# Kernel tuning notes

Measured on AMD Instinct MI355X. Metric: run time of the kernel, lower is better.

## Reference

```python
import jax, jax.numpy as jnp
import numpy as np

# dims
V, D, H = 30000, 300, 300
NS, L = 10000, 32
B, NMAX, MMAX = 256, 128, 128
EPS = 0.1          # sinkhorn entropic regularizer
ITERS = 50         # fixed sinkhorn sweeps (replaces convergence check, jit-friendly)
NEG = 1e9
PAD = 0


def setup_inputs() -> dict:
    key = jax.random.key(0)
    ks = jax.random.split(key, 12)
    data = jax.random.randint(ks[0], (NS, L), 0, V, dtype=jnp.int32)
    row_idx = jax.random.randint(ks[1], (B, NMAX), 0, NS, dtype=jnp.int32)
    col_idx = jax.random.randint(ks[2], (B, MMAX), 0, NS, dtype=jnp.int32)
    row_len = jax.random.randint(ks[3], (B,), 1, NMAX + 1, dtype=jnp.int32)
    col_len = jax.random.randint(ks[4], (B,), 1, MMAX + 1, dtype=jnp.int32)
    g = lambda k, shape, fan: (jax.random.normal(k, shape, jnp.float32) / np.sqrt(fan)).astype(jnp.float32)
    return {
        'data': data, 'row_idx': row_idx, 'col_idx': col_idx,
        'row_len': row_len, 'col_len': col_len,
        'emb': g(ks[5], (V, D), D),
        'W1': g(ks[6], (D, H), D), 'b1': jnp.zeros((H,), jnp.float32),
        'W2': g(ks[7], (H, H), H), 'b2': jnp.zeros((H,), jnp.float32),
        'Wc': g(ks[8], (2 * H, H), 2 * H), 'bc': jnp.zeros((H,), jnp.float32),
        'Wcls': g(ks[9], (2 * H, H), 2 * H), 'bcls': jnp.zeros((H,), jnp.float32),
        'Wout': g(ks[10], (H, 2), H), 'bout': jnp.zeros((2,), jnp.float32),
    }


def _forward(data, row_idx, col_idx, row_len, col_len,
             emb, W1, b1, W2, b2, Wc, bc, Wcls, bcls, Wout, bout):
    # ---- Embedder: token embedding + masked mean pool over tokens ----
    tok = emb[data]                                        # [NS, L, D]
    tmask = (data != PAD).astype(tok.dtype)[..., None]     # [NS, L, 1]
    enc = (tok * tmask).sum(1) / jnp.clip(tmask.sum(1), 1.0)   # [NS, D]
    # ---- attention_forward: 2-layer FFN ----
    henc = jax.nn.relu(jax.nn.relu(enc @ W1 + b1) @ W2 + b2)   # [NS, H]
    # ---- variable-length gather + pad (scope) ----
    rows = henc[row_idx]                                   # [B, NMAX, H]
    cols = henc[col_idx]                                   # [B, MMAX, H]
    rmask = (jnp.arange(NMAX)[None, :] < row_len[:, None]).astype(henc.dtype)
    cmask = (jnp.arange(MMAX)[None, :] < col_len[:, None]).astype(henc.dtype)
    rows = rows * rmask[..., None]
    cols = cols * cmask[..., None]
    # ---- batched pairwise cosine cost ----
    rn = rows / (jnp.linalg.norm(rows, axis=-1, keepdims=True) + 1e-8)
    cn = cols / (jnp.linalg.norm(cols, axis=-1, keepdims=True) + 1e-8)
    C = 1.0 - jnp.einsum('bnd,bmd->bnm', rn, cn)           # [B, NMAX, MMAX]
    pmask = rmask[:, :, None] * cmask[:, None, :]
    Cm = jnp.where(pmask > 0, C, 1e4)
    # uniform marginals over valid rows/cols (log-domain, -inf -> -NEG on pads)
    loga = jnp.where(rmask > 0, -jnp.log(row_len.astype(C.dtype))[:, None], -NEG)
    logb = jnp.where(cmask > 0, -jnp.log(col_len.astype(C.dtype))[:, None], -NEG)
    # ---- log-domain Sinkhorn (row/col marginal rescaling) ----
    def step(carry, _):
        f, g = carry
        f = EPS * loga - EPS * jax.nn.logsumexp((g[:, None, :] - Cm) / EPS, axis=2)
        g = EPS * logb - EPS * jax.nn.logsumexp((f[:, :, None] - Cm) / EPS, axis=1)
        return (f, g), None
    (f, g), _ = jax.lax.scan(step, (jnp.zeros_like(loga), jnp.zeros_like(logb)), None, length=ITERS)
    P = jnp.exp((f[:, :, None] + g[:, None, :] - Cm) / EPS) * pmask  # [B, NMAX, MMAX]
    # ---- attend: column_alignments @ rows, row_alignments @ columns ----
    attended_row = jnp.einsum('bnm,bnd->bmd', P, rows)     # P^T @ rows
    attended_col = jnp.einsum('bnm,bmd->bnd', P, cols)     # P @ cols
    # ---- compare_forward (1 layer) + masked sum ----
    cr = jax.nn.relu(jnp.concatenate([rows, attended_col], -1) @ Wc + bc)
    cr = (cr * rmask[..., None]).sum(1)                    # [B, H]
    cc = jax.nn.relu(jnp.concatenate([cols, attended_row], -1) @ Wc + bc)
    cc = (cc * cmask[..., None]).sum(1)                    # [B, H]
    # ---- cls_forward + out ----
    z = jax.nn.relu(jnp.concatenate([cr, cc], -1) @ Wcls + bcls)
    return z @ Wout + bout                                 # [B, 2]


def reference(data, row_idx, col_idx, row_len, col_len,
              emb, W1, b1, W2, b2, Wc, bc, Wcls, bcls, Wout, bout):
    return _forward(data, row_idx, col_idx, row_len, col_len,
                    emb, W1, b1, W2, b2, Wc, bc, Wcls, bcls, Wout, bout)
```

## Files before the change

kernel.cpp:

```cpp
#include <hip/hip_runtime.h>
#include <math.h>

#define NS 10000
#define LSEQ 32
#define DDIM 300
#define HDIM 300
#define BB 256
#define NMAX 128
#define MMAX 128
#define EPSR 0.1f
#define SITERS 50
#define KPAD 320
#define NPADW 384

typedef __attribute__((ext_vector_type(8))) short bf16x8;
typedef __attribute__((ext_vector_type(4))) float f32x4;

__device__ __forceinline__ ushort f2bf(float x) {
  union { float f; unsigned u; } c; c.f = x;
  unsigned r = (c.u + 0x7fffu + ((c.u >> 16) & 1u)) >> 16;
  return (ushort)r;
}
__device__ __forceinline__ float bf2f(ushort h) {
  union { unsigned u; float f; } c; c.u = ((unsigned)h) << 16;
  return c.f;
}

__global__ __launch_bounds__(256) void k_embed(const int* __restrict__ data,
                                               const float* __restrict__ emb,
                                               ushort* __restrict__ enchi,
                                               ushort* __restrict__ enclo) {
  int wv = threadIdx.x >> 6, lane = threadIdx.x & 63;
  int s = blockIdx.x * 4 + wv;
  int myid = (lane < LSEQ) ? data[s * LSEQ + lane] : 0;
  unsigned long long bal = __ballot(lane < LSEQ && myid != 0);
  int cnt = __popcll(bal);
  const float4* emb4 = (const float4*)emb;
  float4 a0 = make_float4(0.f, 0.f, 0.f, 0.f);
  float4 a1 = make_float4(0.f, 0.f, 0.f, 0.f);
#pragma unroll
  for (int t = 0; t < LSEQ; ++t) {
    int id = __shfl(myid, t, 64);
    float m = (id != 0) ? 1.f : 0.f;
    float4 e0 = emb4[(size_t)id * 75 + lane];
    a0.x += e0.x * m; a0.y += e0.y * m; a0.z += e0.z * m; a0.w += e0.w * m;
    if (lane < 11) {
      float4 e1 = emb4[(size_t)id * 75 + 64 + lane];
      a1.x += e1.x * m; a1.y += e1.y * m; a1.z += e1.z * m; a1.w += e1.w * m;
    }
  }
  float inv = 1.f / (float)(cnt > 0 ? cnt : 1);
  size_t base = (size_t)s * KPAD;
  {
    float v0 = a0.x * inv, v1 = a0.y * inv, v2 = a0.z * inv, v3 = a0.w * inv;
    ushort4 h, l;
    h.x = f2bf(v0); l.x = f2bf(v0 - bf2f(h.x));
    h.y = f2bf(v1); l.y = f2bf(v1 - bf2f(h.y));
    h.z = f2bf(v2); l.z = f2bf(v2 - bf2f(h.z));
    h.w = f2bf(v3); l.w = f2bf(v3 - bf2f(h.w));
    *(ushort4*)&enchi[base + lane * 4] = h;
    *(ushort4*)&enclo[base + lane * 4] = l;
  }
  if (lane < 11) {
    float v0 = a1.x * inv, v1 = a1.y * inv, v2 = a1.z * inv, v3 = a1.w * inv;
    ushort4 h, l;
    h.x = f2bf(v0); l.x = f2bf(v0 - bf2f(h.x));
    h.y = f2bf(v1); l.y = f2bf(v1 - bf2f(h.y));
    h.z = f2bf(v2); l.z = f2bf(v2 - bf2f(h.z));
    h.w = f2bf(v3); l.w = f2bf(v3 - bf2f(h.w));
    *(ushort4*)&enchi[base + 256 + lane * 4] = h;
    *(ushort4*)&enclo[base + 256 + lane * 4] = l;
  } else if (lane < 16) {
    ushort4 z; z.x = z.y = z.z = z.w = 0;
    *(ushort4*)&enchi[base + 300 + (lane - 11) * 4] = z;
    *(ushort4*)&enclo[base + 300 + (lane - 11) * 4] = z;
  }
}

__global__ __launch_bounds__(256) void k_cvt_all(
    const float* __restrict__ W1, const float* __restrict__ W2,
    const float* __restrict__ Wc, ushort* __restrict__ W1hi,
    ushort* __restrict__ W1lo, ushort* __restrict__ W2hi,
    ushort* __restrict__ W2lo, ushort* __restrict__ Wchi,
    ushort* __restrict__ Wclo) {
  int i = blockIdx.x * 256 + threadIdx.x;
  const int SA = NPADW * KPAD;
  const int SC = 640 * KPAD;
  float v = 0.f;
  ushort *ph, *pl;
  int idx;
  if (i < SA) {
    idx = i;
    int n = idx / KPAD, k = idx - n * KPAD;
    if (n < HDIM && k < DDIM) v = W1[(size_t)k * HDIM + n];
    ph = W1hi; pl = W1lo;
  } else if (i < 2 * SA) {
    idx = i - SA;
    int n = idx / KPAD, k = idx - n * KPAD;
    if (n < HDIM && k < HDIM) v = W2[(size_t)k * HDIM + n];
    ph = W2hi; pl = W2lo;
  } else if (i < 2 * SA + SC) {
    idx = i - 2 * SA;
    int n = idx / KPAD, k = idx - n * KPAD;
    if (k < HDIM && n < 2 * HDIM)
      v = (n < HDIM) ? Wc[(size_t)k * HDIM + n]
                     : Wc[(size_t)(HDIM + k) * HDIM + (n - HDIM)];
    ph = Wchi; pl = Wclo;
  } else {
    return;
  }
  ushort h = f2bf(v);
  ph[idx] = h;
  pl[idx] = f2bf(v - bf2f(h));
}

__global__ __launch_bounds__(256) void k_gemm_mfma(
    const ushort* __restrict__ Ahi, const ushort* __restrict__ Alo,
    const ushort* __restrict__ BhiT, const ushort* __restrict__ BloT,
    const float* __restrict__ bias, int M, int N, int relu,
    float* __restrict__ Cf, ushort* __restrict__ Chi,
    ushort* __restrict__ Clo) {
  __shared__ __align__(16) ushort ldsA[2][64][40];
  __shared__ __align__(16) ushort ldsB[2][128][40];
  int tid = threadIdx.x;
  int m0 = blockIdx.x * 64, n0 = blockIdx.y * 128;
  int rowA = tid >> 2, chA = (tid & 3) * 8;
  int rowB = tid >> 1, chB = (tid & 1) * 16;
  bool mok = (m0 + rowA) < M;
  const ushort* pAh = Ahi + (size_t)(m0 + rowA) * KPAD + chA;
  const ushort* pAl = Alo + (size_t)(m0 + rowA) * KPAD + chA;
  const ushort* pBh = BhiT + (size_t)(n0 + rowB) * KPAD + chB;
  const ushort* pBl = BloT + (size_t)(n0 + rowB) * KPAD + chB;
  uint4 rAh, rAl, rBh0, rBh1, rBl0, rBl1;
  uint4 z4; z4.x = z4.y = z4.z = z4.w = 0;
  auto ld = [&](int c) {
    int o = c * 32;
    rAh = mok ? *(const uint4*)(pAh + o) : z4;
    rAl = mok ? *(const uint4*)(pAl + o) : z4;
    rBh0 = *(const uint4*)(pBh + o);
    rBh1 = *(const uint4*)(pBh + o + 8);
    rBl0 = *(const uint4*)(pBl + o);
    rBl1 = *(const uint4*)(pBl + o + 8);
  };
  auto st = [&]() {
    *(uint4*)&ldsA[0][rowA][chA] = rAh;
    *(uint4*)&ldsA[1][rowA][chA] = rAl;
    *(uint4*)&ldsB[0][rowB][chB] = rBh0;
    *(uint4*)&ldsB[0][rowB][chB + 8] = rBh1;
    *(uint4*)&ldsB[1][rowB][chB] = rBl0;
    *(uint4*)&ldsB[1][rowB][chB + 8] = rBl1;
  };
  int w = tid >> 6, lane = tid & 63;
  int q = lane >> 4, l16 = lane & 15;
  int mh = w >> 1, nh = w & 1;
  f32x4 zf = {0.f, 0.f, 0.f, 0.f};
  f32x4 acc[2][4];
#pragma unroll
  for (int s = 0; s < 2; ++s)
#pragma unroll
    for (int t = 0; t < 4; ++t) acc[s][t] = zf;
  ld(0); st(); __syncthreads();
  for (int c = 0; c < 10; ++c) {
    if (c < 9) ld(c + 1);
    bf16x8 ah0 = *(const bf16x8*)&ldsA[0][mh * 32 + l16][q * 8];
    bf16x8 ah1 = *(const bf16x8*)&ldsA[0][mh * 32 + 16 + l16][q * 8];
    bf16x8 al0 = *(const bf16x8*)&ldsA[1][mh * 32 + l16][q * 8];
    bf16x8 al1 = *(const bf16x8*)&ldsA[1][mh * 32 + 16 + l16][q * 8];
#pragma unroll
    for (int t = 0; t < 4; ++t) {
      int brow = nh * 64 + t * 16 + l16;
      bf16x8 bh = *(const bf16x8*)&ldsB[0][brow][q * 8];
      bf16x8 bl = *(const bf16x8*)&ldsB[1][brow][q * 8];
      acc[0][t] = __builtin_amdgcn_mfma_f32_16x16x32_bf16(ah0, bh, acc[0][t], 0, 0, 0);
      acc[0][t] = __builtin_amdgcn_mfma_f32_16x16x32_bf16(ah0, bl, acc[0][t], 0, 0, 0);
      acc[0][t] = __builtin_amdgcn_mfma_f32_16x16x32_bf16(al0, bh, acc[0][t], 0, 0, 0);
      acc[1][t] = __builtin_amdgcn_mfma_f32_16x16x32_bf16(ah1, bh, acc[1][t], 0, 0, 0);
      acc[1][t] = __builtin_amdgcn_mfma_f32_16x16x32_bf16(ah1, bl, acc[1][t], 0, 0, 0);
      acc[1][t] = __builtin_amdgcn_mfma_f32_16x16x32_bf16(al1, bh, acc[1][t], 0, 0, 0);
    }
    __syncthreads();
    if (c < 9) st();
    __syncthreads();
  }
#pragma unroll
  for (int t = 0; t < 4; ++t) {
    int n = n0 + nh * 64 + t * 16 + l16;
    bool nin = n < N;
    float bz = (bias && nin) ? bias[n] : 0.f;
#pragma unroll
    for (int s = 0; s < 2; ++s) {
#pragma unroll
      for (int r = 0; r < 4; ++r) {
        int m = m0 + mh * 32 + s * 16 + q * 4 + r;
        if (m >= M) continue;
        float v = acc[s][t][r] + bz;
        if (relu) v = v > 0.f ? v : 0.f;
        if (Cf && nin) Cf[(size_t)m * N + n] = v;
        if (Chi && n < KPAD) {
          ushort h = 0, l = 0;
          if (nin) { h = f2bf(v); l = f2bf(v - bf2f(h)); }
          Chi[(size_t)m * KPAD + n] = h;
          Clo[(size_t)m * KPAD + n] = l;
        }
      }
    }
  }
}

__global__ __launch_bounds__(256) void k_norm_split(
    const ushort* __restrict__ hehi, const ushort* __restrict__ helo,
    ushort* __restrict__ hnhi, ushort* __restrict__ hnlo) {
  int s = blockIdx.x * 4 + (threadIdx.x >> 6);
  int lane = threadIdx.x & 63;
  if (s >= NS) return;
  const ushort* ph = hehi + (size_t)s * KPAD;
  const ushort* pl = helo + (size_t)s * KPAD;
  float x[5];
  float ss = 0.f;
#pragma unroll
  for (int q = 0; q < 5; ++q) {
    int d = lane + q * 64;
    x[q] = bf2f(ph[d]) + bf2f(pl[d]);
    ss += x[q] * x[q];
  }
#pragma unroll
  for (int off = 32; off > 0; off >>= 1) ss += __shfl_down(ss, off, 64);
  ss = __shfl(ss, 0, 64);
  float inv = 1.f / (sqrtf(ss) + 1e-8f);
  ushort* qh = hnhi + (size_t)s * KPAD;
  ushort* ql = hnlo + (size_t)s * KPAD;
#pragma unroll
  for (int q = 0; q < 5; ++q) {
    int d = lane + q * 64;
    float v = x[q] * inv;
    ushort h = f2bf(v);
    qh[d] = h;
    ql[d] = f2bf(v - bf2f(h));
  }
}

__global__ __launch_bounds__(256) void k_cost_mfma(
    const ushort* __restrict__ hnhi, const ushort* __restrict__ hnlo,
    const int* __restrict__ ridx, const int* __restrict__ cidx,
    const int* __restrict__ rlen, const int* __restrict__ clen,
    float* __restrict__ Kmat) {
  int b = blockIdx.z;
  int r0 = blockIdx.x * 64, c0 = blockIdx.y * 64;
  int rl = rlen[b], cl = clen[b];
  float* Kg = Kmat + (size_t)b * NMAX * MMAX;
  int tid = threadIdx.x;
  if (r0 >= rl || c0 >= cl) {
    for (int l = tid; l < 64 * 16; l += 256) {
      int i = l >> 4, j = (l & 15) << 2;
      *(float4*)&Kg[(size_t)(r0 + i) * MMAX + c0 + j] =
          make_float4(0.f, 0.f, 0.f, 0.f);
    }
    return;
  }
  __shared__ int rix[64], cix[64];
  __shared__ __align__(16) ushort lds[4][64][40];
  if (tid < 64) rix[tid] = ridx[b * NMAX + r0 + tid];
  else if (tid < 128) cix[tid - 64] = cidx[b * MMAX + c0 + tid - 64];
  __syncthreads();
  int row = tid >> 2, ch = tid & 3;
  const ushort* pRh = hnhi + (size_t)rix[row] * KPAD + ch * 8;
  const ushort* pRl = hnlo + (size_t)rix[row] * KPAD + ch * 8;
  const ushort* pCh = hnhi + (size_t)cix[row] * KPAD + ch * 8;
  const ushort* pCl = hnlo + (size_t)cix[row] * KPAD + ch * 8;
  uint4 rRh, rRl, rCh, rCl;
  auto ld = [&](int c) {
    int o = c * 32;
    rRh = *(const uint4*)(pRh + o);
    rRl = *(const uint4*)(pRl + o);
    rCh = *(const uint4*)(pCh + o);
    rCl = *(const uint4*)(pCl + o);
  };
  auto st = [&]() {
    *(uint4*)&lds[0][row][ch * 8] = rRh;
    *(uint4*)&lds[1][row][ch * 8] = rRl;
    *(uint4*)&lds[2][row][ch * 8] = rCh;
    *(uint4*)&lds[3][row][ch * 8] = rCl;
  };
  int w = tid >> 6, lane = tid & 63;
  int q = lane >> 4, l16 = lane & 15;
  int mh = w >> 1, nh = w & 1;
  f32x4 zf = {0.f, 0.f, 0.f, 0.f};
  f32x4 acc[2][2];
#pragma unroll
  for (int s = 0; s < 2; ++s)
#pragma unroll
    for (int t = 0; t < 2; ++t) acc[s][t] = zf;
  ld(0); st(); __syncthreads();
  for (int c = 0; c < 10; ++c) {
    if (c < 9) ld(c + 1);
    bf16x8 ah0 = *(const bf16x8*)&lds[0][mh * 32 + l16][q * 8];
    bf16x8 ah1 = *(const bf16x8*)&lds[0][mh * 32 + 16 + l16][q * 8];
    bf16x8 al0 = *(const bf16x8*)&lds[1][mh * 32 + l16][q * 8];
    bf16x8 al1 = *(const bf16x8*)&lds[1][mh * 32 + 16 + l16][q * 8];
#pragma unroll
    for (int t = 0; t < 2; ++t) {
      int brow = nh * 32 + t * 16 + l16;
      bf16x8 bh = *(const bf16x8*)&lds[2][brow][q * 8];
      bf16x8 bl = *(const bf16x8*)&lds[3][brow][q * 8];
      acc[0][t] = __builtin_amdgcn_mfma_f32_16x16x32_bf16(ah0, bh, acc[0][t], 0, 0, 0);
      acc[0][t] = __builtin_amdgcn_mfma_f32_16x16x32_bf16(ah0, bl, acc[0][t], 0, 0, 0);
      acc[0][t] = __builtin_amdgcn_mfma_f32_16x16x32_bf16(al0, bh, acc[0][t], 0, 0, 0);
      acc[1][t] = __builtin_amdgcn_mfma_f32_16x16x32_bf16(ah1, bh, acc[1][t], 0, 0, 0);
      acc[1][t] = __builtin_amdgcn_mfma_f32_16x16x32_bf16(ah1, bl, acc[1][t], 0, 0, 0);
      acc[1][t] = __builtin_amdgcn_mfma_f32_16x16x32_bf16(al1, bh, acc[1][t], 0, 0, 0);
    }
    __syncthreads();
    if (c < 9) st();
    __syncthreads();
  }
#pragma unroll
  for (int t = 0; t < 2; ++t) {
    int n = c0 + nh * 32 + t * 16 + l16;
#pragma unroll
    for (int s = 0; s < 2; ++s) {
#pragma unroll
      for (int r = 0; r < 4; ++r) {
        int m = r0 + mh * 32 + s * 16 + q * 4 + r;
        float kv = (m < rl && n < cl) ? expf((acc[s][t][r] - 1.f) / EPSR) : 0.f;
        Kg[(size_t)m * MMAX + n] = kv;
      }
    }
  }
}

__global__ __launch_bounds__(512) void k_sinkhorn(
    float* __restrict__ Kmat, const int* __restrict__ rlen,
    const int* __restrict__ clen, ushort* __restrict__ Phi,
    ushort* __restrict__ Plo, ushort* __restrict__ PThi,
    ushort* __restrict__ PTlo) {
  __shared__ __align__(16) float vq[4][36];
  __shared__ __align__(16) float uq[4][36];
  int b = blockIdx.x;
  int tid = threadIdx.x;
  int n = tid >> 2, q = tid & 3;
  int rl = rlen[b], cl = clen[b];
  float* Kg = Kmat + (size_t)b * NMAX * MMAX;
  float kr[32], kt[32];
  const float4* Kg4 = (const float4*)(Kg + (size_t)n * MMAX + 32 * q);
#pragma unroll
  for (int t = 0; t < 8; ++t) *(float4*)&kr[4 * t] = Kg4[t];
#pragma unroll
  for (int j = 0; j < 32; ++j) kt[j] = Kg[(size_t)(32 * q + j) * MMAX + n];
  if (tid < 128) vq[tid >> 5][tid & 31] = (tid < cl) ? 1.f : 0.f;
  float av = (n < rl) ? 1.f / (float)rl : 0.f;
  float bv = (n < cl) ? 1.f / (float)cl : 0.f;
  float un = 0.f;
  __syncthreads();
  for (int it = 0; it < SITERS; ++it) {
    float s = 0.f;
#pragma unroll
    for (int t = 0; t < 8; ++t) {
      float4 vv = *(const float4*)&vq[q][4 * t];
      s += kr[4 * t + 0] * vv.x + kr[4 * t + 1] * vv.y +
           kr[4 * t + 2] * vv.z + kr[4 * t + 3] * vv.w;
    }
    s += __shfl_xor(s, 1, 64);
    s += __shfl_xor(s, 2, 64);
    un = (n < rl) ? av / s : 0.f;
    if (q == 0) uq[n >> 5][n & 31] = un;
    __syncthreads();
    float s2 = 0.f;
#pragma unroll
    for (int t = 0; t < 8; ++t) {
      float4 uu = *(const float4*)&uq[q][4 * t];
      s2 += kt[4 * t + 0] * uu.x + kt[4 * t + 1] * uu.y +
            kt[4 * t + 2] * uu.z + kt[4 * t + 3] * uu.w;
    }
    s2 += __shfl_xor(s2, 1, 64);
    s2 += __shfl_xor(s2, 2, 64);
    float vm = (n < cl) ? bv / s2 : 0.f;
    if (q == 0) vq[n >> 5][n & 31] = vm;
    __syncthreads();
  }
  float vn = vq[n >> 5][n & 31];
  size_t rowoff = (size_t)b * (NMAX * MMAX) + (size_t)n * MMAX + 32 * q;
  {
    uint hw[16], lw[16];
#pragma unroll
    for (int t = 0; t < 16; ++t) {
      float p0 = un * kr[2 * t] * vq[q][2 * t];
      float p1 = un * kr[2 * t + 1] * vq[q][2 * t + 1];
      ushort h0 = f2bf(p0), h1 = f2bf(p1);
      hw[t] = (uint)h0 | ((uint)h1 << 16);
      lw[t] = (uint)f2bf(p0 - bf2f(h0)) | ((uint)f2bf(p1 - bf2f(h1)) << 16);
    }
#pragma unroll
    for (int t4 = 0; t4 < 4; ++t4) {
      uint4 vh = make_uint4(hw[4 * t4], hw[4 * t4 + 1], hw[4 * t4 + 2], hw[4 * t4 + 3]);
      uint4 vl = make_uint4(lw[4 * t4], lw[4 * t4 + 1], lw[4 * t4 + 2], lw[4 * t4 + 3]);
      *(uint4*)(Phi + rowoff + 8 * t4) = vh;
      *(uint4*)(Plo + rowoff + 8 * t4) = vl;
    }
  }
  {
    uint hw[16], lw[16];
#pragma unroll
    for (int t = 0; t < 16; ++t) {
      float p0 = uq[q][2 * t] * kt[2 * t] * vn;
      float p1 = uq[q][2 * t + 1] * kt[2 * t + 1] * vn;
      ushort h0 = f2bf(p0), h1 = f2bf(p1);
      hw[t] = (uint)h0 | ((uint)h1 << 16);
      lw[t] = (uint)f2bf(p0 - bf2f(h0)) | ((uint)f2bf(p1 - bf2f(h1)) << 16);
    }
#pragma unroll
    for (int t4 = 0; t4 < 4; ++t4) {
      uint4 vh = make_uint4(hw[4 * t4], hw[4 * t4 + 1], hw[4 * t4 + 2], hw[4 * t4 + 3]);
      uint4 vl = make_uint4(lw[4 * t4], lw[4 * t4 + 1], lw[4 * t4 + 2], lw[4 * t4 + 3]);
      *(uint4*)(PThi + rowoff + 8 * t4) = vh;
      *(uint4*)(PTlo + rowoff + 8 * t4) = vl;
    }
  }
}

__global__ __launch_bounds__(256) void k_att_mfma(
    const ushort* __restrict__ Phi, const ushort* __restrict__ Plo,
    const ushort* __restrict__ PThi, const ushort* __restrict__ PTlo,
    const float* __restrict__ HcB, const int* __restrict__ row_idx,
    const int* __restrict__ col_idx, const int* __restrict__ row_len,
    const int* __restrict__ col_len, const float* __restrict__ bc,
    float* __restrict__ cr, float* __restrict__ cc) {
  int b = blockIdx.y;
  int side = blockIdx.z;
  int c0 = blockIdx.x * 64;
  const int* idx_main = side == 0 ? row_idx : col_idx;
  const int* idx_other = side == 0 ? col_idx : row_idx;
  int lm = side == 0 ? row_len[b] : col_len[b];
  int lo = side == 0 ? col_len[b] : row_len[b];
  const ushort* Ah = (side == 0 ? Phi : PThi) + (size_t)b * (NMAX * MMAX);
  const ushort* Al = (side == 0 ? Plo : PTlo) + (size_t)b * (NMAX * MMAX);
  float* outacc = side == 0 ? cr : cc;

  __shared__ __align__(16) ushort gldh[64][128];
  __shared__ __align__(16) ushort gldl[64][128];
  __shared__ float red[4][64];
  __shared__ int iox[NMAX];
  __shared__ int imx[NMAX];

  int tid = threadIdx.x;
  int w = tid >> 6, lane = tid & 63;
  int q = lane >> 4, l16 = lane & 15;
  if (tid < 128) iox[tid] = idx_other[b * NMAX + tid];
  else imx[tid - 128] = idx_main[b * NMAX + tid - 128];
  __syncthreads();

  int nkc = (lo + 31) >> 5;
  int ndt = (300 - c0 + 15) >> 4;
  if (ndt > 4) ndt = 4;
  bool dok = (c0 + lane) < 300;

  int i0a = w * 16;
  int i0b = 64 + w * 16;
  bool act0 = i0a < lm;
  bool act1 = i0b < lm;

  float gv[32];
#pragma unroll
  for (int t = 0; t < 32; ++t) {
    int k = w * 32 + t;
    gv[t] = (k < lo && dok) ? HcB[(size_t)iox[k] * 600 + 300 + c0 + lane]
                            : 0.f;
  }
  float mpre[2][4][4];
#pragma unroll
  for (int s = 0; s < 2; ++s) {
    int ib = ((s == 0) ? i0a : i0b) + q * 4;
#pragma unroll
    for (int r = 0; r < 4; ++r) {
      int i = ib + r;
      int hrow = imx[i];
#pragma unroll
      for (int dt = 0; dt < 4; ++dt) {
        int col = c0 + dt * 16 + l16;
        mpre[s][r][dt] =
            (i < lm && col < 300) ? HcB[(size_t)hrow * 600 + col] : 0.f;
      }
    }
  }
  float bcv[4];
#pragma unroll
  for (int dt = 0; dt < 4; ++dt) {
    int col = c0 + dt * 16 + l16;
    bcv[dt] = (col < 300) ? bc[col] : 0.f;
  }

  if (w < nkc) {
#pragma unroll
    for (int blk = 0; blk < 4; ++blk) {
      int kb8 = 4 * w + blk;
      int phys = kb8 ^ (lane & 15);
      ushort hb[8], lb[8];
#pragma unroll
      for (int e = 0; e < 8; ++e) {
        float v = gv[blk * 8 + e];
        ushort h = f2bf(v);
        hb[e] = h;
        lb[e] = f2bf(v - bf2f(h));
      }
      *(uint4*)&gldh[lane][phys * 8] = *(uint4*)hb;
      *(uint4*)&gldl[lane][phys * 8] = *(uint4*)lb;
    }
  }
  __syncthreads();

  f32x4 zf = {0.f, 0.f, 0.f, 0.f};
  f32x4 acc0[4], acc1[4];
#pragma unroll
  for (int dt = 0; dt < 4; ++dt) { acc0[dt] = zf; acc1[dt] = zf; }

#pragma unroll 1
  for (int ch = 0; ch < 2; ++ch) {
    if (ch * 2 >= nkc) break;
    bf16x8 f0h[2], f0l[2], f1h[2], f1l[2];
#pragma unroll
    for (int u = 0; u < 2; ++u) {
      int c = ch * 2 + u;
      if (c < nkc) {
        size_t oa = (size_t)(i0a + l16) * MMAX + 32 * c + 8 * q;
        size_t ob = (size_t)(i0b + l16) * MMAX + 32 * c + 8 * q;
        if (act0) {
          f0h[u] = *(const bf16x8*)&Ah[oa];
          f0l[u] = *(const bf16x8*)&Al[oa];
        }
        if (act1) {
          f1h[u] = *(const bf16x8*)&Ah[ob];
          f1l[u] = *(const bf16x8*)&Al[ob];
        }
      }
    }
#pragma unroll
    for (int u = 0; u < 2; ++u) {
      int c = ch * 2 + u;
      if (c < nkc) {
        int phys = (4 * c + q) ^ l16;
#pragma unroll
        for (int dt = 0; dt < 4; ++dt) {
          if (dt < ndt) {
            int d = dt * 16 + l16;
            bf16x8 bh = *(const bf16x8*)&gldh[d][phys * 8];
            bf16x8 bl = *(const bf16x8*)&gldl[d][phys * 8];
            if (act0) {
              acc0[dt] = __builtin_amdgcn_mfma_f32_16x16x32_bf16(f0h[u], bh, acc0[dt], 0, 0, 0);
              acc0[dt] = __builtin_amdgcn_mfma_f32_16x16x32_bf16(f0h[u], bl, acc0[dt], 0, 0, 0);
              acc0[dt] = __builtin_amdgcn_mfma_f32_16x16x32_bf16(f0l[u], bh, acc0[dt], 0, 0, 0);
            }
            if (act1) {
              acc1[dt] = __builtin_amdgcn_mfma_f32_16x16x32_bf16(f1h[u], bh, acc1[dt], 0, 0, 0);
              acc1[dt] = __builtin_amdgcn_mfma_f32_16x16x32_bf16(f1h[u], bl, acc1[dt], 0, 0, 0);
              acc1[dt] = __builtin_amdgcn_mfma_f32_16x16x32_bf16(f1l[u], bh, acc1[dt], 0, 0, 0);
            }
          }
        }
      }
    }
  }

  float psum[4] = {0.f, 0.f, 0.f, 0.f};
#pragma unroll
  for (int s = 0; s < 2; ++s) {
    bool act = (s == 0) ? act0 : act1;
    if (!act) continue;
    int ibase = ((s == 0) ? i0a : i0b) + q * 4;
#pragma unroll
    for (int r = 0; r < 4; ++r) {
      int i = ibase + r;
      if (i >= lm) continue;
#pragma unroll
      for (int dt = 0; dt < 4; ++dt) {
        int col = c0 + dt * 16 + l16;
        if (dt < ndt && col < 300) {
          float av = (s == 0) ? acc0[dt][r] : acc1[dt][r];
          float y = av + mpre[s][r][dt] + bcv[dt];
          psum[dt] += y > 0.f ? y : 0.f;
        }
      }
    }
  }
#pragma unroll
  for (int dt = 0; dt < 4; ++dt) {
    psum[dt] += __shfl_xor(psum[dt], 16, 64);
    psum[dt] += __shfl_xor(psum[dt], 32, 64);
  }
  if (lane < 16) {
#pragma unroll
    for (int dt = 0; dt < 4; ++dt) red[w][dt * 16 + lane] = psum[dt];
  }
  __syncthreads();
  if (tid < 64) {
    float s = red[0][tid] + red[1][tid] + red[2][tid] + red[3][tid];
    int col = c0 + tid;
    if (col < 300) outacc[(size_t)b * HDIM + col] = s;
  }
}

__global__ __launch_bounds__(320) void k_cls(
    const float* __restrict__ cr, const float* __restrict__ cc,
    const float* __restrict__ Wcls, const float* __restrict__ bcls,
    const float* __restrict__ Wout, const float* __restrict__ bout,
    float* __restrict__ out) {
  __shared__ __align__(16) float cz[2 * HDIM];
  __shared__ float zz[HDIM];
  int b = blockIdx.x, tid = threadIdx.x;
  if (tid < HDIM) {
    cz[tid] = cr[(size_t)b * HDIM + tid];
    cz[HDIM + tid] = cc[(size_t)b * HDIM + tid];
  }
  __syncthreads();
  if (tid < HDIM) {
    float acc = bcls[tid];
    for (int k4 = 0; k4 < 2 * HDIM; k4 += 4) {
      float4 c = *(const float4*)&cz[k4];
      acc += c.x * Wcls[(size_t)(k4 + 0) * HDIM + tid] +
             c.y * Wcls[(size_t)(k4 + 1) * HDIM + tid] +
             c.z * Wcls[(size_t)(k4 + 2) * HDIM + tid] +
             c.w * Wcls[(size_t)(k4 + 3) * HDIM + tid];
    }
    zz[tid] = acc > 0.f ? acc : 0.f;
  }
  __syncthreads();
  int o = tid >> 6, lane = tid & 63;
  if (o < 2) {
    float p = 0.f;
    for (int j = lane; j < HDIM; j += 64) p += zz[j] * Wout[(size_t)j * 2 + o];
#pragma unroll
    for (int off = 32; off > 0; off >>= 1) p += __shfl_down(p, off, 64);
    if (lane == 0) out[b * 2 + o] = p + bout[o];
  }
}

extern "C" void kernel_launch(void* const* d_in, const int* in_sizes, int n_in,
                              void* d_out, int out_size, void* d_ws, size_t ws_size,
                              hipStream_t stream) {
  (void)in_sizes; (void)n_in; (void)out_size; (void)ws_size;
  const int* data = (const int*)d_in[0];
  const int* row_idx = (const int*)d_in[1];
  const int* col_idx = (const int*)d_in[2];
  const int* row_len = (const int*)d_in[3];
  const int* col_len = (const int*)d_in[4];
  const float* emb = (const float*)d_in[5];
  const float* W1 = (const float*)d_in[6];
  const float* b1 = (const float*)d_in[7];
  const float* W2 = (const float*)d_in[8];
  const float* b2 = (const float*)d_in[9];
  const float* Wc = (const float*)d_in[10];
  const float* bc = (const float*)d_in[11];
  const float* Wcls = (const float*)d_in[12];
  const float* bcls = (const float*)d_in[13];
  const float* Wout = (const float*)d_in[14];
  const float* bout = (const float*)d_in[15];
  float* out = (float*)d_out;

  char* wp = (char*)d_ws;
  auto carve = [&](size_t bytes) {
    char* p = wp; wp += (bytes + 255) & ~(size_t)255; return p;
  };
  ushort* enchi = (ushort*)carve((size_t)NS * KPAD * 2);
  ushort* enclo = (ushort*)carve((size_t)NS * KPAD * 2);
  ushort* h1hi = (ushort*)carve((size_t)NS * KPAD * 2);
  ushort* h1lo = (ushort*)carve((size_t)NS * KPAD * 2);
  ushort* hehi = (ushort*)carve((size_t)NS * KPAD * 2);
  ushort* helo = (ushort*)carve((size_t)NS * KPAD * 2);
  ushort* hnhi = (ushort*)carve((size_t)NS * KPAD * 2);
  ushort* hnlo = (ushort*)carve((size_t)NS * KPAD * 2);
  ushort* W1hi = (ushort*)carve((size_t)NPADW * KPAD * 2);
  ushort* W1lo = (ushort*)carve((size_t)NPADW * KPAD * 2);
  ushort* W2hi = (ushort*)carve((size_t)NPADW * KPAD * 2);
  ushort* W2lo = (ushort*)carve((size_t)NPADW * KPAD * 2);
  ushort* Wchi = (ushort*)carve((size_t)640 * KPAD * 2);
  ushort* Wclo = (ushort*)carve((size_t)640 * KPAD * 2);
  float* HcB = (float*)carve((size_t)NS * 600 * 4);
  float* Km = (float*)carve((size_t)BB * NMAX * MMAX * 4);
  float* cr = (float*)carve((size_t)BB * HDIM * 4);
  float* cc = (float*)carve((size_t)BB * HDIM * 4);

  ushort* Phi = enchi;
  ushort* Plo = h1hi;
  ushort* PThi = hehi;
  ushort* PTlo = hnhi;

  int gM = (NS + 63) / 64;
  int cvtTotal = 2 * NPADW * KPAD + 640 * KPAD;

  k_embed<<<NS / 4, 256, 0, stream>>>(data, emb, enchi, enclo);
  k_cvt_all<<<(cvtTotal + 255) / 256, 256, 0, stream>>>(
      W1, W2, Wc, W1hi, W1lo, W2hi, W2lo, Wchi, Wclo);
  k_gemm_mfma<<<dim3(gM, 3), 256, 0, stream>>>(
      enchi, enclo, W1hi, W1lo, b1, NS, HDIM, 1, nullptr, h1hi, h1lo);
  k_gemm_mfma<<<dim3(gM, 3), 256, 0, stream>>>(
      h1hi, h1lo, W2hi, W2lo, b2, NS, HDIM, 1, nullptr, hehi, helo);
  k_norm_split<<<(NS + 3) / 4, 256, 0, stream>>>(hehi, helo, hnhi, hnlo);
  k_gemm_mfma<<<dim3(gM, 5), 256, 0, stream>>>(
      hehi, helo, Wchi, Wclo, nullptr, NS, 2 * HDIM, 0, HcB, nullptr, nullptr);
  k_cost_mfma<<<dim3(2, 2, BB), 256, 0, stream>>>(hnhi, hnlo, row_idx, col_idx,
                                                  row_len, col_len, Km);
  k_sinkhorn<<<BB, 512, 0, stream>>>(Km, row_len, col_len, Phi, Plo, PThi, PTlo);
  k_att_mfma<<<dim3(5, BB, 2), 256, 0, stream>>>(
      Phi, Plo, PThi, PTlo, HcB, row_idx, col_idx, row_len, col_len, bc, cr, cc);
  k_cls<<<BB, 320, 0, stream>>>(cr, cc, Wcls, bcls, Wout, bout, out);
}
```

Measured before the change: 375.7 us.

## Split embedding pooling across column quarters and token halves per block

```diff
diff --git a/kernel.cpp b/kernel.cpp
--- a/kernel.cpp
+++ b/kernel.cpp
@@ -30,50 +30,53 @@
                                                const float* __restrict__ emb,
                                                ushort* __restrict__ enchi,
                                                ushort* __restrict__ enclo) {
+  int bid = blockIdx.x;
+  int q = (bid & 7) >> 1;
+  int p = bid & 1;
+  int g = bid >> 3;
   int wv = threadIdx.x >> 6, lane = threadIdx.x & 63;
-  int s = blockIdx.x * 4 + wv;
+  int s = (g * 2 + p) * 4 + wv;
   int myid = (lane < LSEQ) ? data[s * LSEQ + lane] : 0;
   unsigned long long bal = __ballot(lane < LSEQ && myid != 0);
   int cnt = __popcll(bal);
+  int half = (lane < 19) ? 0 : ((lane < 38) ? 1 : -1);
+  int col = (half == 1) ? lane - 19 : lane;
+  int gcol4 = q * 76 + col * 4;
+  bool act = (half >= 0) && (gcol4 < 300);
+  int c4 = gcol4 >> 2;
   const float4* emb4 = (const float4*)emb;
-  float4 a0 = make_float4(0.f, 0.f, 0.f, 0.f);
-  float4 a1 = make_float4(0.f, 0.f, 0.f, 0.f);
-#pragma unroll
-  for (int t = 0; t < LSEQ; ++t) {
-    int id = __shfl(myid, t, 64);
-    float m = (id != 0) ? 1.f : 0.f;
-    float4 e0 = emb4[(size_t)id * 75 + lane];
-    a0.x += e0.x * m; a0.y += e0.y * m; a0.z += e0.z * m; a0.w += e0.w * m;
-    if (lane < 11) {
-      float4 e1 = emb4[(size_t)id * 75 + 64 + lane];
-      a1.x += e1.x * m; a1.y += e1.y * m; a1.z += e1.z * m; a1.w += e1.w * m;
-    }
-  }
-  float inv = 1.f / (float)(cnt > 0 ? cnt : 1);
-  size_t base = (size_t)s * KPAD;
-  {
-    float v0 = a0.x * inv, v1 = a0.y * inv, v2 = a0.z * inv, v3 = a0.w * inv;
+  float4 a = make_float4(0.f, 0.f, 0.f, 0.f);
+  int tbase = (half == 1) ? 16 : 0;
+#pragma unroll
+  for (int t = 0; t < 16; ++t) {
+    int id = __shfl(myid, tbase + t, 64);
+    if (act && id != 0) {
+      float4 e = emb4[(size_t)id * 75 + c4];
+      a.x += e.x; a.y += e.y; a.z += e.z; a.w += e.w;
+    }
+  }
+  int partner = (lane + 19) & 63;
+  float4 o;
+  o.x = __shfl(a.x, partner, 64);
+  o.y = __shfl(a.y, partner, 64);
+  o.z = __shfl(a.z, partner, 64);
+  o.w = __shfl(a.w, partner, 64);
+  if (lane < 19 && gcol4 < 300) {
+    float inv = 1.f / (float)(cnt > 0 ? cnt : 1);
+    float v0 = (a.x + o.x) * inv, v1 = (a.y + o.y) * inv;
+    float v2 = (a.z + o.z) * inv, v3 = (a.w + o.w) * inv;
     ushort4 h, l;
     h.x = f2bf(v0); l.x = f2bf(v0 - bf2f(h.x));
     h.y = f2bf(v1); l.y = f2bf(v1 - bf2f(h.y));
     h.z = f2bf(v2); l.z = f2bf(v2 - bf2f(h.z));
     h.w = f2bf(v3); l.w = f2bf(v3 - bf2f(h.w));
-    *(ushort4*)&enchi[base + lane * 4] = h;
-    *(ushort4*)&enclo[base + lane * 4] = l;
-  }
-  if (lane < 11) {
-    float v0 = a1.x * inv, v1 = a1.y * inv, v2 = a1.z * inv, v3 = a1.w * inv;
-    ushort4 h, l;
-    h.x = f2bf(v0); l.x = f2bf(v0 - bf2f(h.x));
-    h.y = f2bf(v1); l.y = f2bf(v1 - bf2f(h.y));
-    h.z = f2bf(v2); l.z = f2bf(v2 - bf2f(h.z));
-    h.w = f2bf(v3); l.w = f2bf(v3 - bf2f(h.w));
-    *(ushort4*)&enchi[base + 256 + lane * 4] = h;
-    *(ushort4*)&enclo[base + 256 + lane * 4] = l;
-  } else if (lane < 16) {
+    *(ushort4*)&enchi[(size_t)s * KPAD + gcol4] = h;
+    *(ushort4*)&enclo[(size_t)s * KPAD + gcol4] = l;
+  } else if (q == 3 && lane >= 45 && lane < 50) {
     ushort4 z; z.x = z.y = z.z = z.w = 0;
-    *(ushort4*)&enchi[base + 300 + (lane - 11) * 4] = z;
-    *(ushort4*)&enclo[base + 300 + (lane - 11) * 4] = z;
+    int off = 300 + (lane - 45) * 4;
+    *(ushort4*)&enchi[(size_t)s * KPAD + off] = z;
+    *(ushort4*)&enclo[(size_t)s * KPAD + off] = z;
   }
 }
 
@@ -685,7 +688,7 @@
   int gM = (NS + 63) / 64;
   int cvtTotal = 2 * NPADW * KPAD + 640 * KPAD;
 
-  k_embed<<<NS / 4, 256, 0, stream>>>(data, emb, enchi, enclo);
+  k_embed<<<NS, 256, 0, stream>>>(data, emb, enchi, enclo);
   k_cvt_all<<<(cvtTotal + 255) / 256, 256, 0, stream>>>(
       W1, W2, Wc, W1hi, W1lo, W2hi, W2lo, Wchi, Wclo);
   k_gemm_mfma<<<dim3(gM, 3), 256, 0, stream>>>(
```

Result: faster. 362.4 us (-3.5%).
